# Kernel tuning notes

Measured on AMD Instinct MI355X. Metric: run time of the kernel, lower is better.

Reference implementation:

```python
import jax, jax.numpy as jnp
import numpy as np

P_DROP = 0.5  # F.dropout default


def _afc(x, w, b):
    # Per-sample 1x1 grouped conv == batched matmul over the channel dim.
    # x: [B, Cin, H, W], w: [B, Cout, Cin, 1, 1], b: [B, Cout]
    w2 = w[:, :, :, 0, 0]  # [B, Cout, Cin]
    return jnp.einsum('boi,bihw->bohw', w2, x) + b[:, :, None, None]


def setup_inputs() -> dict:
    key = jax.random.key(0)
    ks = jax.random.split(key, 16)
    B, HW = 64, 8
    dims = [1024, 512, 256, 128, 64, 1]
    inp = {}
    inp['x'] = jax.random.normal(ks[0], (B, dims[0], HW, HW), dtype=jnp.float32)
    for i in range(5):
        cin, cout = dims[i], dims[i + 1]
        scale = 1.0 / np.sqrt(cin).astype(np.float32)
        inp[f'w{i+1}'] = jax.random.normal(ks[1 + 2 * i], (B, cout, cin, 1, 1), dtype=jnp.float32) * scale
        inp[f'b{i+1}'] = jax.random.normal(ks[2 + 2 * i], (B, cout), dtype=jnp.float32) * 0.1
    inp['drop1'] = jax.random.uniform(ks[11], (B, dims[1], HW, HW), dtype=jnp.float32)
    inp['drop2'] = jax.random.uniform(ks[12], (B, dims[2], HW, HW), dtype=jnp.float32)
    return inp


def reference(x, w1, b1, w2, b2, w3, b3, w4, b4, w5, b5, drop1, drop2):
    inv_keep = 1.0 / (1.0 - P_DROP)
    q = jax.nn.sigmoid(_afc(x, w1, b1))
    q = q * (drop1 >= P_DROP).astype(q.dtype) * inv_keep
    q = jax.nn.sigmoid(_afc(q, w2, b2))
    q = q * (drop2 >= P_DROP).astype(q.dtype) * inv_keep
    q = jax.nn.sigmoid(_afc(q, w3, b3))
    q = jax.nn.sigmoid(_afc(q, w4, b4))
    q = _afc(q, w5, b5)  # [B, 1, H, W]
    return jnp.squeeze(q)  # [B, H, W]
```

## Files before the change

### kernel.cpp

```cpp
#include <hip/hip_runtime.h>
#include <hip/hip_bf16.h>


typedef __attribute__((ext_vector_type(4))) float f32x4;
typedef __attribute__((ext_vector_type(8))) short short8;
typedef unsigned short ushort_t;
typedef unsigned int uint_t;

__device__ __forceinline__ void split8(const float (&f)[8], short8& hi, short8& lo) {
#pragma unroll
  for (int i = 0; i < 8; i++) {
    uint_t u = __builtin_bit_cast(uint_t, f[i]);
    hi[i] = (short)(u >> 16);
    float hf = __builtin_bit_cast(float, u & 0xffff0000u);
    float l = f[i] - hf;
    lo[i] = (short)(__builtin_bit_cast(uint_t, l) >> 16);
  }
}

__device__ __forceinline__ void run_gemm(const float* __restrict__ xbase,
                                         const float* __restrict__ wrow,
                                         ushort_t* lds, int Cin,
                                         int wave, int lane, f32x4 acc[4]) {
  const int l15 = lane & 15, l4 = lane >> 4;
  const float* xp = xbase + (wave * 8) * 64 + lane;

  {
    float x0[8];
#pragma unroll
    for (int i = 0; i < 8; i++) x0[i] = xp[i * 64];
    short8 xh, xl;
    split8(x0, xh, xl);
    *(short8*)(lds + 0 * 2560 + lane * 40 + wave * 8) = xh;
    *(short8*)(lds + 1 * 2560 + lane * 40 + wave * 8) = xl;
  }
  f32x4 wv0 = *(const f32x4*)(wrow);
  f32x4 wv1 = *(const f32x4*)(wrow + 4);
  __syncthreads();

  const int ksteps = Cin >> 5;
  int cur = 0;
  for (int ks = 0; ks < ksteps; ks++) {
    const bool more = (ks + 1 < ksteps);
    float xn[8];
    f32x4 wn0, wn1;
    if (more) {
      const float* xp2 = xp + (size_t)(ks + 1) * 2048;
#pragma unroll
      for (int i = 0; i < 8; i++) xn[i] = xp2[i * 64];
      const float* wp2 = wrow + (ks + 1) * 32;
      wn0 = *(const f32x4*)(wp2);
      wn1 = *(const f32x4*)(wp2 + 4);
    }
    float wf[8];
#pragma unroll
    for (int i = 0; i < 4; i++) { wf[i] = wv0[i]; wf[4 + i] = wv1[i]; }
    short8 ahi, alo;
    split8(wf, ahi, alo);

    ushort_t* bh = lds + (cur * 2 + 0) * 2560;
    ushort_t* bl = lds + (cur * 2 + 1) * 2560;
#pragma unroll
    for (int nf = 0; nf < 4; nf++) {
      int off = (nf * 16 + l15) * 40 + l4 * 8;
      short8 bhf = *(const short8*)(bh + off);
      short8 blf = *(const short8*)(bl + off);
      acc[nf] = __builtin_amdgcn_mfma_f32_16x16x32_bf16(ahi, bhf, acc[nf], 0, 0, 0);
      acc[nf] = __builtin_amdgcn_mfma_f32_16x16x32_bf16(ahi, blf, acc[nf], 0, 0, 0);
      acc[nf] = __builtin_amdgcn_mfma_f32_16x16x32_bf16(alo, bhf, acc[nf], 0, 0, 0);
    }
    if (more) {
      short8 xh, xl;
      split8(xn, xh, xl);
      *(short8*)(lds + ((cur ^ 1) * 2 + 0) * 2560 + lane * 40 + wave * 8) = xh;
      *(short8*)(lds + ((cur ^ 1) * 2 + 1) * 2560 + lane * 40 + wave * 8) = xl;
      wv0 = wn0;
      wv1 = wn1;
    }
    __syncthreads();
    cur ^= 1;
  }
}

template <int EPI>
__global__ __launch_bounds__(256, 4) void gemm_layer(
    const float* __restrict__ X, const float* __restrict__ W,
    const float* __restrict__ Bias, const float* __restrict__ Drop,
    float* __restrict__ Out, int Cin, int Cout) {
  const int b = blockIdx.x & 63;
  const int mt = blockIdx.x >> 6;
  const int tid = threadIdx.x, wave = tid >> 6, lane = tid & 63;
  const int l15 = lane & 15, l4 = lane >> 4;
  const int m0 = mt * 64 + wave * 16;
  __shared__ __align__(16) ushort_t lds[2 * 2 * 2560];

  const float* xbase = X + (size_t)b * Cin * 64;
  const float* wrow = W + ((size_t)b * Cout + (m0 + l15)) * (size_t)Cin + l4 * 8;

  f32x4 acc[4];
#pragma unroll
  for (int i = 0; i < 4; i++) acc[i] = {0.f, 0.f, 0.f, 0.f};

  run_gemm(xbase, wrow, lds, Cin, wave, lane, acc);

  const size_t obase = (size_t)b * Cout;
#pragma unroll
  for (int r = 0; r < 4; r++) {
    int o = m0 + l4 * 4 + r;
    float bv = Bias[obase + o];
#pragma unroll
    for (int nf = 0; nf < 4; nf++) {
      int s = nf * 16 + l15;
      float v = acc[nf][r] + bv;
      if (EPI >= 1) v = 1.0f / (1.0f + __expf(-v));
      if (EPI == 2) {
        float dv = Drop[(obase + o) * 64 + s];
        v = (dv >= 0.5f) ? 2.0f * v : 0.0f;
      }
      Out[(obase + o) * 64 + s] = v;
    }
  }
}

__global__ __launch_bounds__(256, 4) void l45_kernel(
    const float* __restrict__ Q3, const float* __restrict__ W4,
    const float* __restrict__ B4f, const float* __restrict__ W5,
    const float* __restrict__ B5f, float* __restrict__ Out) {
  const int b = blockIdx.x;
  const int tid = threadIdx.x, wave = tid >> 6, lane = tid & 63;
  const int l15 = lane & 15, l4 = lane >> 4;
  const int m0 = wave * 16;
  __shared__ __align__(16) ushort_t lds[2 * 2 * 2560];
  __shared__ float q4s[64][64];
  __shared__ float part[4][64];

  const float* xbase = Q3 + (size_t)b * 128 * 64;
  const float* wrow = W4 + ((size_t)b * 64 + (m0 + l15)) * 128 + l4 * 8;

  f32x4 acc[4];
#pragma unroll
  for (int i = 0; i < 4; i++) acc[i] = {0.f, 0.f, 0.f, 0.f};

  run_gemm(xbase, wrow, lds, 128, wave, lane, acc);

#pragma unroll
  for (int r = 0; r < 4; r++) {
    int o = m0 + l4 * 4 + r;
    float bv = B4f[b * 64 + o];
#pragma unroll
    for (int nf = 0; nf < 4; nf++) {
      float v = acc[nf][r] + bv;
      v = 1.0f / (1.0f + __expf(-v));
      q4s[o][nf * 16 + l15] = v;
    }
  }
  __syncthreads();

  {
    float a = 0.f;
#pragma unroll
    for (int k = wave * 16; k < wave * 16 + 16; k++)
      a += W5[b * 64 + k] * q4s[k][lane];
    part[wave][lane] = a;
  }
  __syncthreads();
  if (wave == 0) {
    Out[b * 64 + lane] =
        part[0][lane] + part[1][lane] + part[2][lane] + part[3][lane] + B5f[b];
  }
}

extern "C" void kernel_launch(void* const* d_in, const int* in_sizes, int n_in,
                              void* d_out, int out_size, void* d_ws, size_t ws_size,
                              hipStream_t stream) {
  const float* x = (const float*)d_in[0];
  const float* w1 = (const float*)d_in[1];
  const float* b1 = (const float*)d_in[2];
  const float* w2 = (const float*)d_in[3];
  const float* b2 = (const float*)d_in[4];
  const float* w3 = (const float*)d_in[5];
  const float* b3 = (const float*)d_in[6];
  const float* w4 = (const float*)d_in[7];
  const float* b4 = (const float*)d_in[8];
  const float* w5 = (const float*)d_in[9];
  const float* b5 = (const float*)d_in[10];
  const float* drop1 = (const float*)d_in[11];
  const float* drop2 = (const float*)d_in[12];
  float* out = (float*)d_out;

  float* q1 = (float*)d_ws;
  float* q2 = q1 + (size_t)64 * 512 * 64;
  float* q3 = q2 + (size_t)64 * 256 * 64;

  gemm_layer<2><<<dim3(8 * 64), 256, 0, stream>>>(x, w1, b1, drop1, q1, 1024, 512);
  gemm_layer<2><<<dim3(4 * 64), 256, 0, stream>>>(q1, w2, b2, drop2, q2, 512, 256);
  gemm_layer<1><<<dim3(2 * 64), 256, 0, stream>>>(q2, w3, b3, nullptr, q3, 256, 128);
  l45_kernel<<<dim3(64), 256, 0, stream>>>(q3, w4, b4, w5, b5, out);
}
```

Before: 304.5 us.

## Fuse layers 3-5 into one kernel and deepen weight prefetch to two steps

Layer 3 GEMM is merged with layers 4 and 5 into one per-batch kernel. Each wave now computes two 16-row M tiles, and the layer-3 result stays in LDS instead of round-tripping through global memory. The GEMM loop prefetches weights two k-steps ahead and uses sched_barriers to keep loads ahead of the MFMAs. Launch bounds drop to 2 waves per EU for more registers. The fused kernel runs only 64 blocks, which lowers parallelism for layer 3.

```diff
diff --git a/kernel.cpp b/kernel.cpp
--- a/kernel.cpp
+++ b/kernel.cpp
@@ -18,6 +18,8 @@
   }
 }
 
+#define MFMA_BF16 __builtin_amdgcn_mfma_f32_16x16x32_bf16
+
 __device__ __forceinline__ void run_gemm(const float* __restrict__ xbase,
                                          const float* __restrict__ wrow,
                                          ushort_t* lds, int Cin,
@@ -34,27 +36,37 @@
     *(short8*)(lds + 0 * 2560 + lane * 40 + wave * 8) = xh;
     *(short8*)(lds + 1 * 2560 + lane * 40 + wave * 8) = xl;
   }
-  f32x4 wv0 = *(const f32x4*)(wrow);
-  f32x4 wv1 = *(const f32x4*)(wrow + 4);
-  __syncthreads();
-
   const int ksteps = Cin >> 5;
+  f32x4 wA0 = *(const f32x4*)(wrow);
+  f32x4 wA1 = *(const f32x4*)(wrow + 4);
+  f32x4 wB0{}, wB1{};
+  if (ksteps > 1) {
+    wB0 = *(const f32x4*)(wrow + 32);
+    wB1 = *(const f32x4*)(wrow + 36);
+  }
+  __syncthreads();
+
   int cur = 0;
   for (int ks = 0; ks < ksteps; ks++) {
-    const bool more = (ks + 1 < ksteps);
+    const bool morex = (ks + 1 < ksteps);
+    const bool morew = (ks + 2 < ksteps);
     float xn[8];
-    f32x4 wn0, wn1;
-    if (more) {
+    f32x4 wn0{}, wn1{};
+    if (morex) {
       const float* xp2 = xp + (size_t)(ks + 1) * 2048;
 #pragma unroll
       for (int i = 0; i < 8; i++) xn[i] = xp2[i * 64];
-      const float* wp2 = wrow + (ks + 1) * 32;
+    }
+    if (morew) {
+      const float* wp2 = wrow + (ks + 2) * 32;
       wn0 = *(const f32x4*)(wp2);
       wn1 = *(const f32x4*)(wp2 + 4);
     }
+    __builtin_amdgcn_sched_barrier(0);
+
     float wf[8];
 #pragma unroll
-    for (int i = 0; i < 4; i++) { wf[i] = wv0[i]; wf[4 + i] = wv1[i]; }
+    for (int i = 0; i < 4; i++) { wf[i] = wA0[i]; wf[4 + i] = wA1[i]; }
     short8 ahi, alo;
     split8(wf, ahi, alo);
 
@@ -65,25 +77,26 @@
       int off = (nf * 16 + l15) * 40 + l4 * 8;
       short8 bhf = *(const short8*)(bh + off);
       short8 blf = *(const short8*)(bl + off);
-      acc[nf] = __builtin_amdgcn_mfma_f32_16x16x32_bf16(ahi, bhf, acc[nf], 0, 0, 0);
-      acc[nf] = __builtin_amdgcn_mfma_f32_16x16x32_bf16(ahi, blf, acc[nf], 0, 0, 0);
-      acc[nf] = __builtin_amdgcn_mfma_f32_16x16x32_bf16(alo, bhf, acc[nf], 0, 0, 0);
-    }
-    if (more) {
+      acc[nf] = MFMA_BF16(ahi, bhf, acc[nf], 0, 0, 0);
+      acc[nf] = MFMA_BF16(ahi, blf, acc[nf], 0, 0, 0);
+      acc[nf] = MFMA_BF16(alo, bhf, acc[nf], 0, 0, 0);
+    }
+    __builtin_amdgcn_sched_barrier(0);
+
+    if (morex) {
       short8 xh, xl;
       split8(xn, xh, xl);
       *(short8*)(lds + ((cur ^ 1) * 2 + 0) * 2560 + lane * 40 + wave * 8) = xh;
       *(short8*)(lds + ((cur ^ 1) * 2 + 1) * 2560 + lane * 40 + wave * 8) = xl;
-      wv0 = wn0;
-      wv1 = wn1;
-    }
+    }
+    wA0 = wB0; wA1 = wB1; wB0 = wn0; wB1 = wn1;
     __syncthreads();
     cur ^= 1;
   }
 }
 
 template <int EPI>
-__global__ __launch_bounds__(256, 4) void gemm_layer(
+__global__ __launch_bounds__(256, 2) void gemm_layer(
     const float* __restrict__ X, const float* __restrict__ W,
     const float* __restrict__ Bias, const float* __restrict__ Drop,
     float* __restrict__ Out, int Cin, int Cout) {
@@ -112,7 +125,7 @@
     for (int nf = 0; nf < 4; nf++) {
       int s = nf * 16 + l15;
       float v = acc[nf][r] + bv;
-      if (EPI >= 1) v = 1.0f / (1.0f + __expf(-v));
+      v = 1.0f / (1.0f + __expf(-v));
       if (EPI == 2) {
         float dv = Drop[(obase + o) * 64 + s];
         v = (dv >= 0.5f) ? 2.0f * v : 0.0f;
@@ -122,36 +135,163 @@
   }
 }
 
-__global__ __launch_bounds__(256, 4) void l45_kernel(
-    const float* __restrict__ Q3, const float* __restrict__ W4,
-    const float* __restrict__ B4f, const float* __restrict__ W5,
-    const float* __restrict__ B5f, float* __restrict__ Out) {
+__global__ __launch_bounds__(256, 2) void l345_kernel(
+    const float* __restrict__ Q2, const float* __restrict__ W3,
+    const float* __restrict__ B3, const float* __restrict__ W4,
+    const float* __restrict__ B4, const float* __restrict__ W5,
+    const float* __restrict__ B5, float* __restrict__ Out) {
   const int b = blockIdx.x;
   const int tid = threadIdx.x, wave = tid >> 6, lane = tid & 63;
   const int l15 = lane & 15, l4 = lane >> 4;
-  const int m0 = wave * 16;
+
   __shared__ __align__(16) ushort_t lds[2 * 2 * 2560];
-  __shared__ float q4s[64][64];
+  __shared__ __align__(16) float q3s[64][132];
+  __shared__ __align__(16) float q4s[64][68];
   __shared__ float part[4][64];
 
-  const float* xbase = Q3 + (size_t)b * 128 * 64;
-  const float* wrow = W4 + ((size_t)b * 64 + (m0 + l15)) * 128 + l4 * 8;
-
-  f32x4 acc[4];
-#pragma unroll
-  for (int i = 0; i < 4; i++) acc[i] = {0.f, 0.f, 0.f, 0.f};
-
-  run_gemm(xbase, wrow, lds, 128, wave, lane, acc);
-
-#pragma unroll
-  for (int r = 0; r < 4; r++) {
-    int o = m0 + l4 * 4 + r;
-    float bv = B4f[b * 64 + o];
-#pragma unroll
-    for (int nf = 0; nf < 4; nf++) {
-      float v = acc[nf][r] + bv;
-      v = 1.0f / (1.0f + __expf(-v));
-      q4s[o][nf * 16 + l15] = v;
+  const float* xbase = Q2 + (size_t)b * 256 * 64;
+  const float* wrow0 = W3 + ((size_t)b * 128 + wave * 32 + l15) * 256 + l4 * 8;
+  const float* wrow1 = wrow0 + 16 * 256;
+  const float* xp = xbase + (wave * 8) * 64 + lane;
+
+  f32x4 acc3[2][4];
+#pragma unroll
+  for (int m = 0; m < 2; m++)
+#pragma unroll
+    for (int i = 0; i < 4; i++) acc3[m][i] = {0.f, 0.f, 0.f, 0.f};
+
+  {
+    float x0[8];
+#pragma unroll
+    for (int i = 0; i < 8; i++) x0[i] = xp[i * 64];
+    short8 xh, xl;
+    split8(x0, xh, xl);
+    *(short8*)(lds + 0 * 2560 + lane * 40 + wave * 8) = xh;
+    *(short8*)(lds + 1 * 2560 + lane * 40 + wave * 8) = xl;
+  }
+  f32x4 wA00 = *(const f32x4*)(wrow0), wA01 = *(const f32x4*)(wrow0 + 4);
+  f32x4 wA10 = *(const f32x4*)(wrow1), wA11 = *(const f32x4*)(wrow1 + 4);
+  f32x4 wB00 = *(const f32x4*)(wrow0 + 32), wB01 = *(const f32x4*)(wrow0 + 36);
+  f32x4 wB10 = *(const f32x4*)(wrow1 + 32), wB11 = *(const f32x4*)(wrow1 + 36);
+  __syncthreads();
+
+  int cur = 0;
+  for (int ks = 0; ks < 8; ks++) {
+    const bool morex = (ks + 1 < 8), morew = (ks + 2 < 8);
+    float xn[8];
+    f32x4 wn00{}, wn01{}, wn10{}, wn11{};
+    if (morex) {
+      const float* xp2 = xp + (size_t)(ks + 1) * 2048;
+#pragma unroll
+      for (int i = 0; i < 8; i++) xn[i] = xp2[i * 64];
+    }
+    if (morew) {
+      const float* p0 = wrow0 + (ks + 2) * 32;
+      const float* p1 = wrow1 + (ks + 2) * 32;
+      wn00 = *(const f32x4*)(p0); wn01 = *(const f32x4*)(p0 + 4);
+      wn10 = *(const f32x4*)(p1); wn11 = *(const f32x4*)(p1 + 4);
+    }
+    __builtin_amdgcn_sched_barrier(0);
+
+    float wf0[8], wf1[8];
+#pragma unroll
+    for (int i = 0; i < 4; i++) {
+      wf0[i] = wA00[i]; wf0[4 + i] = wA01[i];
+      wf1[i] = wA10[i]; wf1[4 + i] = wA11[i];
+    }
+    short8 a0h, a0l, a1h, a1l;
+    split8(wf0, a0h, a0l);
+    split8(wf1, a1h, a1l);
+
+    ushort_t* bh = lds + (cur * 2 + 0) * 2560;
+    ushort_t* bl = lds + (cur * 2 + 1) * 2560;
+#pragma unroll
+    for (int nf = 0; nf < 4; nf++) {
+      int off = (nf * 16 + l15) * 40 + l4 * 8;
+      short8 bhf = *(const short8*)(bh + off);
+      short8 blf = *(const short8*)(bl + off);
+      acc3[0][nf] = MFMA_BF16(a0h, bhf, acc3[0][nf], 0, 0, 0);
+      acc3[0][nf] = MFMA_BF16(a0h, blf, acc3[0][nf], 0, 0, 0);
+      acc3[0][nf] = MFMA_BF16(a0l, bhf, acc3[0][nf], 0, 0, 0);
+      acc3[1][nf] = MFMA_BF16(a1h, bhf, acc3[1][nf], 0, 0, 0);
+      acc3[1][nf] = MFMA_BF16(a1h, blf, acc3[1][nf], 0, 0, 0);
+      acc3[1][nf] = MFMA_BF16(a1l, bhf, acc3[1][nf], 0, 0, 0);
+    }
+    __builtin_amdgcn_sched_barrier(0);
+
+    if (morex) {
+      short8 xh, xl;
+      split8(xn, xh, xl);
+      *(short8*)(lds + ((cur ^ 1) * 2 + 0) * 2560 + lane * 40 + wave * 8) = xh;
+      *(short8*)(lds + ((cur ^ 1) * 2 + 1) * 2560 + lane * 40 + wave * 8) = xl;
+    }
+    wA00 = wB00; wA01 = wB01; wA10 = wB10; wA11 = wB11;
+    wB00 = wn00; wB01 = wn01; wB10 = wn10; wB11 = wn11;
+    __syncthreads();
+    cur ^= 1;
+  }
+
+  const float* w4row = W4 + ((size_t)b * 64 + wave * 16 + l15) * 128 + l4 * 8;
+  f32x4 w4r[8];
+#pragma unroll
+  for (int ss = 0; ss < 4; ss++) {
+    w4r[2 * ss] = *(const f32x4*)(w4row + ss * 32);
+    w4r[2 * ss + 1] = *(const f32x4*)(w4row + ss * 32 + 4);
+  }
+
+#pragma unroll
+  for (int mf = 0; mf < 2; mf++) {
+    int o0 = wave * 32 + mf * 16 + l4 * 4;
+#pragma unroll
+    for (int nf = 0; nf < 4; nf++) {
+      int s = nf * 16 + l15;
+      f32x4 v;
+#pragma unroll
+      for (int r = 0; r < 4; r++) {
+        float t = acc3[mf][nf][r] + B3[(size_t)b * 128 + o0 + r];
+        v[r] = 1.0f / (1.0f + __expf(-t));
+      }
+      *(f32x4*)&q3s[s][o0] = v;
+    }
+  }
+  __syncthreads();
+
+  f32x4 acc4[4];
+#pragma unroll
+  for (int i = 0; i < 4; i++) acc4[i] = {0.f, 0.f, 0.f, 0.f};
+
+#pragma unroll
+  for (int ks = 0; ks < 4; ks++) {
+    float wf[8];
+#pragma unroll
+    for (int i = 0; i < 4; i++) { wf[i] = w4r[2 * ks][i]; wf[4 + i] = w4r[2 * ks + 1][i]; }
+    short8 ah, al;
+    split8(wf, ah, al);
+#pragma unroll
+    for (int nf = 0; nf < 4; nf++) {
+      int s = nf * 16 + l15;
+      float bf[8];
+      *(f32x4*)&bf[0] = *(const f32x4*)&q3s[s][ks * 32 + l4 * 8];
+      *(f32x4*)&bf[4] = *(const f32x4*)&q3s[s][ks * 32 + l4 * 8 + 4];
+      short8 bhf, blf;
+      split8(bf, bhf, blf);
+      acc4[nf] = MFMA_BF16(ah, bhf, acc4[nf], 0, 0, 0);
+      acc4[nf] = MFMA_BF16(ah, blf, acc4[nf], 0, 0, 0);
+      acc4[nf] = MFMA_BF16(al, bhf, acc4[nf], 0, 0, 0);
+    }
+  }
+  {
+    int o0 = wave * 16 + l4 * 4;
+#pragma unroll
+    for (int nf = 0; nf < 4; nf++) {
+      int s = nf * 16 + l15;
+      f32x4 v;
+#pragma unroll
+      for (int r = 0; r < 4; r++) {
+        float t = acc4[nf][r] + B4[(size_t)b * 64 + o0 + r];
+        v[r] = 1.0f / (1.0f + __expf(-t));
+      }
+      *(f32x4*)&q4s[s][o0] = v;
     }
   }
   __syncthreads();
@@ -160,13 +300,13 @@
     float a = 0.f;
 #pragma unroll
     for (int k = wave * 16; k < wave * 16 + 16; k++)
-      a += W5[b * 64 + k] * q4s[k][lane];
+      a += W5[(size_t)b * 64 + k] * q4s[lane][k];
     part[wave][lane] = a;
   }
   __syncthreads();
   if (wave == 0) {
-    Out[b * 64 + lane] =
-        part[0][lane] + part[1][lane] + part[2][lane] + part[3][lane] + B5f[b];
+    Out[(size_t)b * 64 + lane] =
+        part[0][lane] + part[1][lane] + part[2][lane] + part[3][lane] + B5[b];
   }
 }
 
@@ -190,10 +330,8 @@
 
   float* q1 = (float*)d_ws;
   float* q2 = q1 + (size_t)64 * 512 * 64;
-  float* q3 = q2 + (size_t)64 * 256 * 64;
 
   gemm_layer<2><<<dim3(8 * 64), 256, 0, stream>>>(x, w1, b1, drop1, q1, 1024, 512);
   gemm_layer<2><<<dim3(4 * 64), 256, 0, stream>>>(q1, w2, b2, drop2, q2, 512, 256);
-  gemm_layer<1><<<dim3(2 * 64), 256, 0, stream>>>(q2, w3, b3, nullptr, q3, 256, 128);
-  l45_kernel<<<dim3(64), 256, 0, stream>>>(q3, w4, b4, w5, b5, out);
-}
+  l345_kernel<<<dim3(64), 256, 0, stream>>>(q2, w3, b3, w4, b4, w5, b5, out);
+}
```

Measured after the change: 295.5 us. -2.9%, faster.
